# Kernel tuning notes

Hardware: AMD Instinct MI355X
Metric: run time of the kernel (lower is better)

## Reference

```python
import jax, jax.numpy as jnp
import numpy as np

B, S, IN_DIM = 16, 1024, 64
D, H, FF, L, OUT = 512, 8, 2048, 6, 256
HD = D // H
EPS = 1e-5


def _ln(x, g, b):
    m = jnp.mean(x, axis=-1, keepdims=True)
    v = jnp.var(x, axis=-1, keepdims=True)
    return (x - m) * jax.lax.rsqrt(v + EPS) * g + b


def setup_inputs() -> dict:
    key = jax.random.key(0)
    ks = jax.random.split(key, 24)
    def rn(k, shape, scale=0.02):
        return jax.random.normal(k, shape, dtype=jnp.float32) * scale
    return {
        "x": jax.random.normal(ks[0], (B, S, IN_DIM), dtype=jnp.float32),
        "in_w": rn(ks[1], (IN_DIM, D)), "in_b": jnp.zeros((D,), jnp.float32),
        "in_ln_g": jnp.ones((D,), jnp.float32), "in_ln_b": jnp.zeros((D,), jnp.float32),
        "pos": rn(ks[2], (S, D)),
        "qkv_w": rn(ks[3], (L, D, 3 * D)), "qkv_b": jnp.zeros((L, 3 * D), jnp.float32),
        "ao_w": rn(ks[4], (L, D, D)), "ao_b": jnp.zeros((L, D), jnp.float32),
        "ff_w1": rn(ks[5], (L, D, FF)), "ff_b1": jnp.zeros((L, FF), jnp.float32),
        "ff_w2": rn(ks[6], (L, FF, D)), "ff_b2": jnp.zeros((L, D), jnp.float32),
        "ln1_g": jnp.ones((L, D), jnp.float32), "ln1_b": jnp.zeros((L, D), jnp.float32),
        "ln2_g": jnp.ones((L, D), jnp.float32), "ln2_b": jnp.zeros((L, D), jnp.float32),
        "o_w1": rn(ks[7], (D, D // 2)), "o_b1": jnp.zeros((D // 2,), jnp.float32),
        "o_ln_g": jnp.ones((D // 2,), jnp.float32), "o_ln_b": jnp.zeros((D // 2,), jnp.float32),
        "o_w2": rn(ks[8], (D // 2, OUT)), "o_b2": jnp.zeros((OUT,), jnp.float32),
    }


def reference(x, in_w, in_b, in_ln_g, in_ln_b, pos,
              qkv_w, qkv_b, ao_w, ao_b, ff_w1, ff_b1, ff_w2, ff_b2,
              ln1_g, ln1_b, ln2_g, ln2_b,
              o_w1, o_b1, o_ln_g, o_ln_b, o_w2, o_b2):
    h = x @ in_w + in_b                      # [B,S,D]
    h = _ln(h, in_ln_g, in_ln_b)
    h = h + pos[None, :, :]
    scale = 1.0 / jnp.sqrt(jnp.float32(HD))
    for l in range(L):
        qkv = h @ qkv_w[l] + qkv_b[l]        # [B,S,3D]
        q, k, v = jnp.split(qkv, 3, axis=-1)
        q = q.reshape(B, S, H, HD)
        k = k.reshape(B, S, H, HD)
        v = v.reshape(B, S, H, HD)
        scores = jnp.einsum('bqhd,bkhd->bhqk', q, k) * scale
        attn = jax.nn.softmax(scores, axis=-1)
        ctx = jnp.einsum('bhqk,bkhd->bqhd', attn, v).reshape(B, S, D)
        attn_out = ctx @ ao_w[l] + ao_b[l]
        h = _ln(h + attn_out, ln1_g[l], ln1_b[l])
        ff = jax.nn.gelu(h @ ff_w1[l] + ff_b1[l], approximate=False) @ ff_w2[l] + ff_b2[l]
        h = _ln(h + ff, ln2_g[l], ln2_b[l])
    pooled = jnp.mean(h, axis=1)             # [B,D]
    z = jax.nn.gelu(pooled @ o_w1 + o_b1, approximate=False)
    z = _ln(z, o_ln_g, o_ln_b)
    return z @ o_w2 + o_b2                   # [B,OUT]
```

## Files before the change

### kernel.cpp

```cpp
#include <hip/hip_runtime.h>
#include <hip/hip_bf16.h>

#define B_ 16
#define S_ 1024
#define IN_ 64
#define D_ 512
#define H_ 8
#define HD_ 64
#define FF_ 2048
#define L_ 6
#define OUT_ 256
#define BS_ (B_*S_)

typedef __attribute__((ext_vector_type(8))) short s16x8;
typedef __attribute__((ext_vector_type(4))) short s16x4;
typedef __attribute__((ext_vector_type(4))) float f32x4;

#define AS1(p) ((const __attribute__((address_space(1))) void*)(p))
#define AS3(p) ((__attribute__((address_space(3))) void*)(p))

__device__ __forceinline__ ushort f2bf(float x) {
  __hip_bfloat16 h = __float2bfloat16(x);
  return *reinterpret_cast<ushort*>(&h);
}
__device__ __forceinline__ float bf2f(ushort u) {
  unsigned v = ((unsigned)u) << 16;
  union { unsigned u; float f; } c; c.u = v; return c.f;
}
__device__ __forceinline__ float gelu_exact(float x) {
  return 0.5f * x * (1.0f + erff(x * 0.70710678118654752f));
}

template<int BN, int WM, int WN, int MODE>
__global__ __launch_bounds__(256)
void gemm_bt(const ushort* __restrict__ A, int lda,
             const ushort* __restrict__ Bt, int ldb,
             const float* __restrict__ bias,
             ushort* __restrict__ C, int ldc,
             int K)
{
  constexpr int BM = 128;
  constexpr int BK = 64;
  constexpr int FM = BM / (WM * 16);
  constexpr int FN = BN / (WN * 16);
  __shared__ ushort As[BM * BK];
  __shared__ ushort Bs[BN * BK];

  const int tid = threadIdx.x;
  const int lane = tid & 63;
  const int wave = tid >> 6;
  const int wr = wave / WN;
  const int wc = wave % WN;
  const int lrow = lane & 15;
  const int lk = (lane >> 4) * 8;

  const int gx = gridDim.x;
  const int nwg = gx * gridDim.y;
  const int flat = blockIdx.y * gx + blockIdx.x;
  const int T = (flat & 7) * (nwg >> 3) + (flat >> 3);
  const int m0 = (T / gx) * BM;
  const int n0 = (T % gx) * BN;

  f32x4 acc[FM][FN];
#pragma unroll
  for (int m = 0; m < FM; ++m)
#pragma unroll
    for (int n = 0; n < FN; ++n)
      acc[m][n] = (f32x4){0.f, 0.f, 0.f, 0.f};

  for (int k0 = 0; k0 < K; k0 += BK) {
    __syncthreads();
#pragma unroll
    for (int rr = 0; rr < BM / 32; ++rr) {
      int c = rr * 256 + tid;
      int row = c >> 3, cg = c & 7;
      __builtin_amdgcn_global_load_lds(
          AS1(A + (size_t)(m0 + row) * lda + k0 + cg * 8),
          AS3(As + (size_t)(rr * 256 + wave * 64) * 8), 16, 0, 0);
    }
#pragma unroll
    for (int rr = 0; rr < BN / 32; ++rr) {
      int c = rr * 256 + tid;
      int row = c >> 3, cg = c & 7;
      __builtin_amdgcn_global_load_lds(
          AS1(Bt + (size_t)(n0 + row) * ldb + k0 + cg * 8),
          AS3(Bs + (size_t)(rr * 256 + wave * 64) * 8), 16, 0, 0);
    }
    __syncthreads();
#pragma unroll
    for (int kk = 0; kk < 2; ++kk) {
      s16x8 a[FM], b[FN];
#pragma unroll
      for (int m = 0; m < FM; ++m)
        a[m] = *(const s16x8*)&As[(wr * FM * 16 + m * 16 + lrow) * BK + kk * 32 + lk];
#pragma unroll
      for (int n = 0; n < FN; ++n)
        b[n] = *(const s16x8*)&Bs[(wc * FN * 16 + n * 16 + lrow) * BK + kk * 32 + lk];
#pragma unroll
      for (int m = 0; m < FM; ++m)
#pragma unroll
        for (int n = 0; n < FN; ++n)
          acc[m][n] = __builtin_amdgcn_mfma_f32_16x16x32_bf16(a[m], b[n], acc[m][n], 0, 0, 0);
    }
  }

  const int rb = m0 + wr * FM * 16 + (lane >> 4) * 4;
  const int cb = n0 + wc * FN * 16 + lrow;
#pragma unroll
  for (int n = 0; n < FN; ++n) {
    int col = cb + n * 16;
    float bv = bias ? bias[col] : 0.0f;
#pragma unroll
    for (int m = 0; m < FM; ++m) {
      int row = rb + m * 16;
#pragma unroll
      for (int r = 0; r < 4; ++r) {
        float v = acc[m][n][r] + bv;
        size_t idx = (size_t)(row + r) * ldc + col;
        if (MODE == 1) C[idx] = f2bf(v);
        else           C[idx] = f2bf(gelu_exact(v));
      }
    }
  }
}

__global__ __launch_bounds__(256)
void flash_kernel(const ushort* __restrict__ qkv, const ushort* __restrict__ vt,
                  ushort* __restrict__ ctx)
{
  constexpr int KB = 128;
  const float KE = 0.125f * 1.44269504f;
  __shared__ ushort ks[KB][72];
  __shared__ ushort vs[HD_][KB + 8];
  const int tid = threadIdx.x;
  const int lane = tid & 63;
  const int wave = tid >> 6;
  const int lrow = lane & 15;
  const int g = lane >> 4;
  const int lk = g * 8;

  const int flat = blockIdx.y * 16 + blockIdx.x;
  const int T = (flat & 7) * 256 + (flat >> 3);
  const int bh = T >> 4;
  const int b = bh >> 3, h = bh & 7;
  const int q0 = (T & 15) * 64;

  s16x8 qf[2];
  {
    const ushort* qrow = qkv + ((size_t)(b * S_ + q0 + wave * 16 + lrow)) * (3 * D_) + h * HD_;
    s16x8 r0 = *(const s16x8*)(qrow + lk);
    s16x8 r1 = *(const s16x8*)(qrow + 32 + lk);
#pragma unroll
    for (int j = 0; j < 8; ++j) {
      qf[0][j] = (short)f2bf(bf2f((ushort)r0[j]) * KE);
      qf[1][j] = (short)f2bf(bf2f((ushort)r1[j]) * KE);
    }
  }
  float lsum = 0.f;
  f32x4 o[4] = {};

  for (int kt = 0; kt < S_ / KB; ++kt) {
    __syncthreads();
    for (int c = tid; c < KB * 8; c += 256) {
      int row = c >> 3, cg = c & 7;
      *(s16x8*)&ks[row][cg * 8] =
          *(const s16x8*)(qkv + ((size_t)(b * S_ + kt * KB + row)) * (3 * D_) + D_ + h * HD_ + cg * 8);
    }
    for (int c = tid; c < HD_ * 16; c += 256) {
      int row = c >> 4, cg = c & 15;
      *(s16x8*)&vs[row][cg * 8] =
          *(const s16x8*)(vt + ((size_t)(bh * HD_ + row)) * S_ + kt * KB + cg * 8);
    }
    __syncthreads();

#pragma unroll
    for (int tp = 0; tp < 4; ++tp) {
      f32x4 s0 = {}, s1 = {};
      {
        s16x8 k00 = *(const s16x8*)&ks[tp * 32 + lrow][lk];
        s16x8 k01 = *(const s16x8*)&ks[tp * 32 + lrow][32 + lk];
        s16x8 k10 = *(const s16x8*)&ks[tp * 32 + 16 + lrow][lk];
        s16x8 k11 = *(const s16x8*)&ks[tp * 32 + 16 + lrow][32 + lk];
        s0 = __builtin_amdgcn_mfma_f32_16x16x32_bf16(k00, qf[0], s0, 0, 0, 0);
        s0 = __builtin_amdgcn_mfma_f32_16x16x32_bf16(k01, qf[1], s0, 0, 0, 0);
        s1 = __builtin_amdgcn_mfma_f32_16x16x32_bf16(k10, qf[0], s1, 0, 0, 0);
        s1 = __builtin_amdgcn_mfma_f32_16x16x32_bf16(k11, qf[1], s1, 0, 0, 0);
      }
      s16x8 pa;
#pragma unroll
      for (int r = 0; r < 4; ++r) {
        float p0 = exp2f(s0[r]);
        float p1 = exp2f(s1[r]);
        lsum += p0 + p1;
        pa[r] = (short)f2bf(p0);
        pa[4 + r] = (short)f2bf(p1);
      }
#pragma unroll
      for (int n2 = 0; n2 < 4; ++n2) {
        const ushort* vr = &vs[n2 * 16 + lrow][tp * 32 + g * 4];
        s16x4 v0 = *(const s16x4*)vr;
        s16x4 v1 = *(const s16x4*)(vr + 16);
        s16x8 vf;
#pragma unroll
        for (int j = 0; j < 4; ++j) { vf[j] = v0[j]; vf[4 + j] = v1[j]; }
        o[n2] = __builtin_amdgcn_mfma_f32_16x16x32_bf16(vf, pa, o[n2], 0, 0, 0);
      }
    }
  }
  lsum += __shfl_xor(lsum, 16);
  lsum += __shfl_xor(lsum, 32);
  float inv = 1.0f / lsum;

  ushort* crow = ctx + ((size_t)(b * S_ + q0 + wave * 16 + lrow)) * D_ + h * HD_;
#pragma unroll
  for (int n2 = 0; n2 < 4; ++n2) {
    s16x4 w;
#pragma unroll
    for (int r = 0; r < 4; ++r) w[r] = (short)f2bf(o[n2][r] * inv);
    *(s16x4*)(crow + n2 * 16 + g * 4) = w;
  }
}

__global__ __launch_bounds__(256)
void ln512_kernel(const ushort* __restrict__ a, const ushort* __restrict__ res,
                  const float* __restrict__ g, const float* __restrict__ bt,
                  const float* __restrict__ pos,
                  ushort* __restrict__ hout)
{
  const int row = blockIdx.x;
  const int t = threadIdx.x;
  const size_t base = (size_t)row * D_;
  float x0 = bf2f(a[base + t]), x1 = bf2f(a[base + t + 256]);
  if (res) { x0 += bf2f(res[base + t]); x1 += bf2f(res[base + t + 256]); }
  float s = x0 + x1, q = x0 * x0 + x1 * x1;
#pragma unroll
  for (int m = 32; m > 0; m >>= 1) { s += __shfl_xor(s, m); q += __shfl_xor(q, m); }
  __shared__ float red[8];
  if ((t & 63) == 0) { red[(t >> 6) * 2] = s; red[(t >> 6) * 2 + 1] = q; }
  __syncthreads();
  s = red[0] + red[2] + red[4] + red[6];
  q = red[1] + red[3] + red[5] + red[7];
  float mean = s * (1.0f / D_);
  float var = q * (1.0f / D_) - mean * mean;
  float rs = rsqrtf(var + 1e-5f);
  float y0 = (x0 - mean) * rs * g[t] + bt[t];
  float y1 = (x1 - mean) * rs * g[t + 256] + bt[t + 256];
  if (pos) {
    int sp = row & (S_ - 1);
    y0 += pos[(size_t)sp * D_ + t];
    y1 += pos[(size_t)sp * D_ + t + 256];
  }
  hout[base + t] = f2bf(y0);
  hout[base + t + 256] = f2bf(y1);
}

__global__ __launch_bounds__(256)
void vtrans_kernel(const ushort* __restrict__ qkv, ushort* __restrict__ vt)
{
  __shared__ ushort tile[64][72];
  const int bh = blockIdx.x;
  const int b = bh >> 3, h = bh & 7;
  const int k0 = blockIdx.y * 64;
  const int t = threadIdx.x;
  for (int c = t; c < 512; c += 256) {
    int row = c >> 3, dg = c & 7;
    *(s16x8*)&tile[row][dg * 8] =
        *(const s16x8*)(qkv + (size_t)(b * S_ + k0 + row) * (3 * D_) + 2 * D_ + h * HD_ + dg * 8);
  }
  __syncthreads();
  int d = t >> 2, kg = t & 3;
  ushort out[16];
#pragma unroll
  for (int j = 0; j < 16; ++j) out[j] = tile[kg * 16 + j][d];
  size_t obase = ((size_t)bh * HD_ + d) * S_ + k0 + kg * 16;
  *(s16x8*)&vt[obase] = *(s16x8*)&out[0];
  *(s16x8*)&vt[obase + 8] = *(s16x8*)&out[8];
}

__global__ void wtrans_kernel(const float* __restrict__ W, ushort* __restrict__ Wt, int K, int N)
{
  __shared__ float tile[32][33];
  int n0 = blockIdx.x * 32, k0 = blockIdx.y * 32;
  int tx = threadIdx.x, ty = threadIdx.y;
#pragma unroll
  for (int r = 0; r < 4; ++r)
    tile[ty * 4 + r][tx] = W[(size_t)(k0 + ty * 4 + r) * N + n0 + tx];
  __syncthreads();
#pragma unroll
  for (int r = 0; r < 4; ++r)
    Wt[(size_t)(n0 + ty * 4 + r) * K + k0 + tx] = f2bf(tile[tx][ty * 4 + r]);
}

__global__ void castx_kernel(const float* __restrict__ x, ushort* __restrict__ xb, int n)
{
  int i = blockIdx.x * blockDim.x + threadIdx.x;
  if (i < n) xb[i] = f2bf(x[i]);
}

__global__ __launch_bounds__(256)
void pool_partial_kernel(const ushort* __restrict__ h, float* __restrict__ pp)
{
  int b = blockIdx.x, ch = blockIdx.y;
  int t = threadIdx.x;
  float s0 = 0, s1 = 0;
  for (int r = 0; r < 128; ++r) {
    size_t base = ((size_t)b * S_ + ch * 128 + r) * D_;
    s0 += bf2f(h[base + t]);
    s1 += bf2f(h[base + t + 256]);
  }
  pp[(size_t)(b * 8 + ch) * D_ + t] = s0;
  pp[(size_t)(b * 8 + ch) * D_ + t + 256] = s1;
}

__global__ __launch_bounds__(256)
void head_kernel(const float* __restrict__ pp,
                 const float* __restrict__ w1, const float* __restrict__ b1,
                 const float* __restrict__ lg, const float* __restrict__ lb,
                 const float* __restrict__ w2, const float* __restrict__ b2,
                 float* __restrict__ out)
{
  __shared__ float pooled[D_];
  __shared__ float z[256];
  int b = blockIdx.x, t = threadIdx.x;
  for (int i = t; i < D_; i += 256) {
    float s = 0;
    for (int c = 0; c < 8; ++c) s += pp[(size_t)(b * 8 + c) * D_ + i];
    pooled[i] = s * (1.0f / S_);
  }
  __syncthreads();
  float acc = 0;
  for (int k = 0; k < D_; ++k) acc += pooled[k] * w1[(size_t)k * 256 + t];
  float zz = gelu_exact(acc + b1[t]);
  float s = zz, q = zz * zz;
#pragma unroll
  for (int m = 32; m > 0; m >>= 1) { s += __shfl_xor(s, m); q += __shfl_xor(q, m); }
  __shared__ float red[8];
  if ((t & 63) == 0) { red[(t >> 6) * 2] = s; red[(t >> 6) * 2 + 1] = q; }
  __syncthreads();
  s = red[0] + red[2] + red[4] + red[6];
  q = red[1] + red[3] + red[5] + red[7];
  float mean = s * (1.0f / 256), var = q * (1.0f / 256) - mean * mean;
  float rs = rsqrtf(var + 1e-5f);
  z[t] = (zz - mean) * rs * lg[t] + lb[t];
  __syncthreads();
  float o = 0;
  for (int k = 0; k < 256; ++k) o += z[k] * w2[(size_t)k * 256 + t];
  out[(size_t)b * 256 + t] = o + b2[t];
}

extern "C" void kernel_launch(void* const* d_in, const int* in_sizes, int n_in,
                              void* d_out, int out_size, void* d_ws, size_t ws_size,
                              hipStream_t stream)
{
  const float* x       = (const float*)d_in[0];
  const float* in_w    = (const float*)d_in[1];
  const float* in_b    = (const float*)d_in[2];
  const float* in_ln_g = (const float*)d_in[3];
  const float* in_ln_b = (const float*)d_in[4];
  const float* pos     = (const float*)d_in[5];
  const float* qkv_w   = (const float*)d_in[6];
  const float* qkv_b   = (const float*)d_in[7];
  const float* ao_w    = (const float*)d_in[8];
  const float* ao_b    = (const float*)d_in[9];
  const float* ff_w1   = (const float*)d_in[10];
  const float* ff_b1   = (const float*)d_in[11];
  const float* ff_w2   = (const float*)d_in[12];
  const float* ff_b2   = (const float*)d_in[13];
  const float* ln1_g   = (const float*)d_in[14];
  const float* ln1_b   = (const float*)d_in[15];
  const float* ln2_g   = (const float*)d_in[16];
  const float* ln2_b   = (const float*)d_in[17];
  const float* o_w1    = (const float*)d_in[18];
  const float* o_b1    = (const float*)d_in[19];
  const float* o_ln_g  = (const float*)d_in[20];
  const float* o_ln_b  = (const float*)d_in[21];
  const float* o_w2    = (const float*)d_in[22];
  const float* o_b2    = (const float*)d_in[23];

  char* wp = (char*)d_ws;
  auto alloc = [&](size_t bytes) {
    char* p = wp;
    wp += (bytes + 255) & ~(size_t)255;
    return p;
  };
  ushort* hb     = (ushort*)alloc((size_t)BS_ * D_ * 2);
  ushort* tmpb   = (ushort*)alloc((size_t)BS_ * D_ * 2);
  ushort* big    = (ushort*)alloc((size_t)BS_ * FF_ * 2);
  ushort* ctxb   = (ushort*)alloc((size_t)BS_ * D_ * 2);
  ushort* xb     = (ushort*)alloc((size_t)BS_ * IN_ * 2);
  ushort* vt     = (ushort*)alloc((size_t)B_ * H_ * HD_ * S_ * 2);
  float*  pp     = (float*) alloc((size_t)B_ * 8 * D_ * 4);
  ushort* in_wt  = (ushort*)alloc((size_t)D_ * IN_ * 2);
  ushort* qkv_wt = (ushort*)alloc((size_t)L_ * 3 * D_ * D_ * 2);
  ushort* ao_wt  = (ushort*)alloc((size_t)L_ * D_ * D_ * 2);
  ushort* ff1_wt = (ushort*)alloc((size_t)L_ * FF_ * D_ * 2);
  ushort* ff2_wt = (ushort*)alloc((size_t)L_ * D_ * FF_ * 2);
  (void)ws_size; (void)n_in; (void)in_sizes; (void)out_size;

  dim3 wb(32, 8);
  wtrans_kernel<<<dim3(D_ / 32, IN_ / 32), wb, 0, stream>>>(in_w, in_wt, IN_, D_);
  for (int l = 0; l < L_; ++l) {
    wtrans_kernel<<<dim3(3 * D_ / 32, D_ / 32), wb, 0, stream>>>(
        qkv_w + (size_t)l * D_ * 3 * D_, qkv_wt + (size_t)l * 3 * D_ * D_, D_, 3 * D_);
    wtrans_kernel<<<dim3(D_ / 32, D_ / 32), wb, 0, stream>>>(
        ao_w + (size_t)l * D_ * D_, ao_wt + (size_t)l * D_ * D_, D_, D_);
    wtrans_kernel<<<dim3(FF_ / 32, D_ / 32), wb, 0, stream>>>(
        ff_w1 + (size_t)l * D_ * FF_, ff1_wt + (size_t)l * FF_ * D_, D_, FF_);
    wtrans_kernel<<<dim3(D_ / 32, FF_ / 32), wb, 0, stream>>>(
        ff_w2 + (size_t)l * FF_ * D_, ff2_wt + (size_t)l * D_ * FF_, FF_, D_);
  }
  castx_kernel<<<BS_ * IN_ / 256, 256, 0, stream>>>(x, xb, BS_ * IN_);

  gemm_bt<128, 2, 2, 1><<<dim3(D_ / 128, BS_ / 128), 256, 0, stream>>>(
      xb, IN_, in_wt, IN_, in_b, tmpb, D_, IN_);
  ln512_kernel<<<BS_, 256, 0, stream>>>(tmpb, nullptr, in_ln_g, in_ln_b, pos, hb);

  for (int l = 0; l < L_; ++l) {
    gemm_bt<128, 2, 2, 1><<<dim3(3 * D_ / 128, BS_ / 128), 256, 0, stream>>>(
        hb, D_, qkv_wt + (size_t)l * 3 * D_ * D_, D_, qkv_b + (size_t)l * 3 * D_,
        big, 3 * D_, D_);
    vtrans_kernel<<<dim3(B_ * H_, S_ / 64), 256, 0, stream>>>(big, vt);
    flash_kernel<<<dim3(S_ / 64, B_ * H_), 256, 0, stream>>>(big, vt, ctxb);
    gemm_bt<128, 2, 2, 1><<<dim3(D_ / 128, BS_ / 128), 256, 0, stream>>>(
        ctxb, D_, ao_wt + (size_t)l * D_ * D_, D_, ao_b + (size_t)l * D_,
        tmpb, D_, D_);
    ln512_kernel<<<BS_, 256, 0, stream>>>(tmpb, hb, ln1_g + (size_t)l * D_,
                                          ln1_b + (size_t)l * D_, nullptr, hb);
    gemm_bt<128, 2, 2, 2><<<dim3(FF_ / 128, BS_ / 128), 256, 0, stream>>>(
        hb, D_, ff1_wt + (size_t)l * FF_ * D_, D_, ff_b1 + (size_t)l * FF_,
        big, FF_, D_);
    gemm_bt<128, 2, 2, 1><<<dim3(D_ / 128, BS_ / 128), 256, 0, stream>>>(
        big, FF_, ff2_wt + (size_t)l * D_ * FF_, FF_, ff_b2 + (size_t)l * D_,
        tmpb, D_, FF_);
    ln512_kernel<<<BS_, 256, 0, stream>>>(tmpb, hb, ln2_g + (size_t)l * D_,
                                          ln2_b + (size_t)l * D_, nullptr, hb);
  }
  pool_partial_kernel<<<dim3(B_, 8), 256, 0, stream>>>(hb, pp);
  head_kernel<<<B_, 256, 0, stream>>>(pp, o_w1, o_b1, o_ln_g, o_ln_b, o_w2, o_b2,
                                      (float*)d_out);
}
```

Baseline: 1.950 ms.

## Swizzle V tile in LDS for flash attention and batch weight transposes

```diff
diff --git a/kernel.cpp b/kernel.cpp
--- a/kernel.cpp
+++ b/kernel.cpp
@@ -131,7 +131,7 @@
   constexpr int KB = 128;
   const float KE = 0.125f * 1.44269504f;
   __shared__ ushort ks[KB][72];
-  __shared__ ushort vs[HD_][KB + 8];
+  __shared__ ushort vs[HD_ * KB];
   const int tid = threadIdx.x;
   const int lane = tid & 63;
   const int wave = tid >> 6;
@@ -168,7 +168,7 @@
     }
     for (int c = tid; c < HD_ * 16; c += 256) {
       int row = c >> 4, cg = c & 15;
-      *(s16x8*)&vs[row][cg * 8] =
+      *(s16x8*)&vs[row * KB + 8 * (cg ^ (row & 7))] =
           *(const s16x8*)(vt + ((size_t)(bh * HD_ + row)) * S_ + kt * KB + cg * 8);
     }
     __syncthreads();
@@ -197,9 +197,13 @@
       }
 #pragma unroll
       for (int n2 = 0; n2 < 4; ++n2) {
-        const ushort* vr = &vs[n2 * 16 + lrow][tp * 32 + g * 4];
-        s16x4 v0 = *(const s16x4*)vr;
-        s16x4 v1 = *(const s16x4*)(vr + 16);
+        int row = n2 * 16 + lrow;
+        int r7 = lrow & 7;
+        int chA = tp * 4 + (g >> 1);
+        int chB = chA + 2;
+        int sub = (g & 1) * 4;
+        s16x4 v0 = *(const s16x4*)&vs[row * KB + 8 * (chA ^ r7) + sub];
+        s16x4 v1 = *(const s16x4*)&vs[row * KB + 8 * (chB ^ r7) + sub];
         s16x8 vf;
 #pragma unroll
         for (int j = 0; j < 4; ++j) { vf[j] = v0[j]; vf[4 + j] = v1[j]; }
@@ -280,15 +284,17 @@
 __global__ void wtrans_kernel(const float* __restrict__ W, ushort* __restrict__ Wt, int K, int N)
 {
   __shared__ float tile[32][33];
+  const float* Wl = W + (size_t)blockIdx.z * K * N;
+  ushort* Wtl = Wt + (size_t)blockIdx.z * K * N;
   int n0 = blockIdx.x * 32, k0 = blockIdx.y * 32;
   int tx = threadIdx.x, ty = threadIdx.y;
 #pragma unroll
   for (int r = 0; r < 4; ++r)
-    tile[ty * 4 + r][tx] = W[(size_t)(k0 + ty * 4 + r) * N + n0 + tx];
+    tile[ty * 4 + r][tx] = Wl[(size_t)(k0 + ty * 4 + r) * N + n0 + tx];
   __syncthreads();
 #pragma unroll
   for (int r = 0; r < 4; ++r)
-    Wt[(size_t)(n0 + ty * 4 + r) * K + k0 + tx] = f2bf(tile[tx][ty * 4 + r]);
+    Wtl[(size_t)(n0 + ty * 4 + r) * K + k0 + tx] = f2bf(tile[tx][ty * 4 + r]);
 }
 
 __global__ void castx_kernel(const float* __restrict__ x, ushort* __restrict__ xb, int n)
@@ -398,17 +404,11 @@
   (void)ws_size; (void)n_in; (void)in_sizes; (void)out_size;
 
   dim3 wb(32, 8);
-  wtrans_kernel<<<dim3(D_ / 32, IN_ / 32), wb, 0, stream>>>(in_w, in_wt, IN_, D_);
-  for (int l = 0; l < L_; ++l) {
-    wtrans_kernel<<<dim3(3 * D_ / 32, D_ / 32), wb, 0, stream>>>(
-        qkv_w + (size_t)l * D_ * 3 * D_, qkv_wt + (size_t)l * 3 * D_ * D_, D_, 3 * D_);
-    wtrans_kernel<<<dim3(D_ / 32, D_ / 32), wb, 0, stream>>>(
-        ao_w + (size_t)l * D_ * D_, ao_wt + (size_t)l * D_ * D_, D_, D_);
-    wtrans_kernel<<<dim3(FF_ / 32, D_ / 32), wb, 0, stream>>>(
-        ff_w1 + (size_t)l * D_ * FF_, ff1_wt + (size_t)l * FF_ * D_, D_, FF_);
-    wtrans_kernel<<<dim3(D_ / 32, FF_ / 32), wb, 0, stream>>>(
-        ff_w2 + (size_t)l * FF_ * D_, ff2_wt + (size_t)l * D_ * FF_, FF_, D_);
-  }
+  wtrans_kernel<<<dim3(D_ / 32, IN_ / 32, 1), wb, 0, stream>>>(in_w, in_wt, IN_, D_);
+  wtrans_kernel<<<dim3(3 * D_ / 32, D_ / 32, L_), wb, 0, stream>>>(qkv_w, qkv_wt, D_, 3 * D_);
+  wtrans_kernel<<<dim3(D_ / 32, D_ / 32, L_), wb, 0, stream>>>(ao_w, ao_wt, D_, D_);
+  wtrans_kernel<<<dim3(FF_ / 32, D_ / 32, L_), wb, 0, stream>>>(ff_w1, ff1_wt, D_, FF_);
+  wtrans_kernel<<<dim3(D_ / 32, FF_ / 32, L_), wb, 0, stream>>>(ff_w2, ff2_wt, FF_, D_);
   castx_kernel<<<BS_ * IN_ / 256, 256, 0, stream>>>(x, xb, BS_ * IN_);
 
   gemm_bt<128, 2, 2, 1><<<dim3(D_ / 128, BS_ / 128), 256, 0, stream>>>(
```

New measurement: 1.931 ms. About the same (-1.0%).
